# Optimization experiments

Hardware: AMD Instinct MI355X
Metric: run time of the kernel (lower is better)

Reference implementation:

```python
import jax, jax.numpy as jnp
import numpy as np

B = 1024     # number of graphs
NMAX = 128   # max nodes per graph (sizes alternate 128/64 -> total 98304 nodes)
D = 128      # feature dim == UOTPooling.dim
NUM = 4      # Bregman-ADMM iterations
EPS = 1e-8
NEG = -1e9   # masked log-value


def setup_inputs() -> dict:
    key = jax.random.key(0)
    ks = jax.random.split(key, 6)
    sizes = np.where(np.arange(B) % 2 == 0, 128, 64)
    batch = jnp.asarray(np.repeat(np.arange(B), sizes), dtype=jnp.int32)  # (98304,)
    T = int(sizes.sum())
    x = jax.random.normal(ks[0], (T, D), dtype=jnp.float32)
    W1 = jax.random.normal(ks[1], (2 * D, D), dtype=jnp.float32) / np.sqrt(D)
    W2 = jax.random.normal(ks[2], (1, 2 * D), dtype=jnp.float32) / np.sqrt(2 * D)
    a1_raw = 0.1 * jax.random.normal(ks[3], (1, 1), dtype=jnp.float32)
    a2_raw = 0.1 * jax.random.normal(ks[4], (1, 1), dtype=jnp.float32)
    a3_raw = 0.1 * jax.random.normal(ks[5], (1, 1), dtype=jnp.float32)
    return {"x": x, "batch": batch, "W1": W1, "W2": W2,
            "a1_raw": a1_raw, "a2_raw": a2_raw, "a3_raw": a3_raw}


def _segment_softmax(scores, batch):
    # torch_geometric.utils.softmax over ragged segments, numerically stable
    m = jax.ops.segment_max(scores, batch, num_segments=B)
    e = jnp.exp(scores - m[batch])
    s = jax.ops.segment_sum(e, batch, num_segments=B)
    return e / (s[batch] + 1e-16)


def _to_dense_batch(v, batch):
    # scatter flat (T, ...) node values into dense (B, NMAX, ...) + validity mask
    T = v.shape[0]
    counts = jax.ops.segment_sum(jnp.ones((T,), jnp.int32), batch, num_segments=B)
    starts = jnp.cumsum(counts) - counts
    pos = jnp.arange(T, dtype=jnp.int32) - starts[batch]
    dense = jnp.zeros((B, NMAX) + v.shape[1:], v.dtype).at[batch, pos].set(v)
    mask = jnp.zeros((B, NMAX), dtype=bool).at[batch, pos].set(True)
    return dense, mask


def _uot_badmm(xd, p0, q0, a1, a2, a3, mask3):
    # log-domain Bregman-ADMM for entropic unbalanced OT ("badmm-e").
    # T: (B, N, D); row marginal (sum over D) ~ eta (samples), column marginal
    # (sum over N) ~ mu (dims); eta, mu softly tied to priors q0, p0 via KL.
    log_p0 = jnp.log(p0 + EPS)                       # (B, 1, D)
    log_q0 = jnp.log(q0 + EPS)                       # (B, N, 1)
    log_t = jnp.where(mask3, log_q0 + log_p0, NEG)   # (B, N, D)
    log_s = log_t
    log_mu = log_p0                                   # (B, 1, D)
    log_eta = jnp.where(mask3, log_q0, NEG)           # (B, N, 1)
    z = jnp.zeros_like(log_t)
    z1 = jnp.zeros_like(log_mu)
    z2 = jnp.zeros_like(log_eta)
    for _ in range(NUM):
        # T-update: each valid row of T sums to eta (softmax over feature dim)
        y = (xd - z) / a1 + log_s
        log_t = jnp.where(mask3, log_eta + jax.nn.log_softmax(y, axis=2), NEG)
        # S-update: each column of S sums to mu (masked softmax over node dim)
        y = jnp.where(mask3, z / a1 + log_t, NEG)
        log_s = jnp.where(mask3, log_mu + jax.nn.log_softmax(y, axis=1), NEG)
        # closed-form KL-prox updates of the unbalanced marginals
        log_cs = jax.scipy.special.logsumexp(log_s, axis=1, keepdims=True)  # (B,1,D)
        log_mu = (a1 * log_cs + a2 * log_p0 - z1) / (a1 + a2)
        log_rt = jax.scipy.special.logsumexp(log_t, axis=2, keepdims=True)  # (B,N,1)
        log_eta = jnp.where(mask3, (a1 * log_rt + a3 * log_q0 - z2) / (a1 + a3), NEG)
        # dual ascent
        z = z + a1 * (jnp.exp(log_t) - jnp.exp(log_s))
        z1 = z1 + a1 * (jnp.exp(log_mu) - jnp.exp(log_cs))
        z2 = z2 + a1 * (jnp.exp(log_eta) - jnp.exp(log_rt))
    return jnp.exp(log_t)


def reference(x, batch, W1, W2, a1_raw, a2_raw, a3_raw):
    # attention scores -> segment softmax -> sample-marginal prior q0
    scores = jnp.tanh(x @ W1.T) @ W2.T               # (T, 1)
    q0_flat = _segment_softmax(scores, batch)        # (T, 1)
    xd, mask = _to_dense_batch(x, batch)             # (B, NMAX, D), (B, NMAX)
    q0, _ = _to_dense_batch(q0_flat, batch)          # (B, NMAX, 1)
    mask3 = mask[:, :, None]                         # (B, NMAX, 1)
    p0 = jnp.full((B, 1, D), 1.0 / D, dtype=x.dtype)
    a1 = jax.nn.softplus(a1_raw)[0, 0]
    a2 = jax.nn.softplus(a2_raw)[0, 0]
    a3 = jax.nn.softplus(a3_raw)[0, 0]
    trans = _uot_badmm(xd, p0, q0, a1, a2, a3, mask3)  # (B, NMAX, D)
    frot = D * xd * trans * mask3
    return jnp.sum(frot, axis=1)                     # (B, D)
```

## Files before the change

### kernel.cpp

```cpp
#include <hip/hip_runtime.h>
#include <hip/hip_bf16.h>
#include <math.h>

#define NEGC -1000000000.0f

using f32x2 = __attribute__((ext_vector_type(2))) float;
using f32x4 = __attribute__((ext_vector_type(4))) float;
using s16x8 = __attribute__((ext_vector_type(8))) short;

__device__ __forceinline__ float softplusf(float v){ return log1pf(expf(v)); }
__device__ __forceinline__ float frcp(float v){ return __builtin_amdgcn_rcpf(v); }
__device__ __forceinline__ short bfs(float f){
  __hip_bfloat16 h = __float2bfloat16(f);
  short s; __builtin_memcpy(&s, &h, 2); return s;
}

__device__ __forceinline__ float addx32(float v){
#if __has_builtin(__builtin_amdgcn_permlane32_swap)
  auto r = __builtin_amdgcn_permlane32_swap(__float_as_uint(v), __float_as_uint(v), false, false);
  return v + __uint_as_float(r[1]);
#else
  return v + __shfl_xor(v, 32, 64);
#endif
}
__device__ __forceinline__ float addx16(float v){
#if __has_builtin(__builtin_amdgcn_permlane16_swap)
  auto r = __builtin_amdgcn_permlane16_swap(__float_as_uint(v), __float_as_uint(v), false, false);
  return v + __uint_as_float(r[1]);
#else
  return v + __shfl_xor(v, 16, 64);
#endif
}
__device__ __forceinline__ float addx8(float v){
  int s = __builtin_amdgcn_update_dpp(0, __float_as_int(v), 0x128, 0xF, 0xF, true);
  return v + __int_as_float(s);
}
__device__ __forceinline__ float addq1(float v){
  int s = __builtin_amdgcn_update_dpp(0, __float_as_int(v), 0xB1, 0xF, 0xF, true);
  return v + __int_as_float(s);
}
__device__ __forceinline__ float addq2(float v){
  int s = __builtin_amdgcn_update_dpp(0, __float_as_int(v), 0x4E, 0xF, 0xF, true);
  return v + __int_as_float(s);
}

__global__ __launch_bounds__(256) void k_prep(const float* __restrict__ W1,
                                              short* __restrict__ wpack,
                                              const int* __restrict__ batch,
                                              int* __restrict__ starts, int T, int Bn,
                                              int* __restrict__ cnt,
                                              int* __restrict__ bigs,
                                              int* __restrict__ smalls){
  const int bx  = blockIdx.x;
  const int tid = threadIdx.x;
  if (bx < 16){
    int gid  = bx * 256 + tid;
    int lane = gid & 63;
    int ft   = gid >> 6;
    int kt   = ft >> 2;
    int dt   = ft & 3;
    const float* src = W1 + (size_t)(kt * 16 + (lane & 15)) * 128 + dt * 32 + (lane >> 4) * 8;
    short o[8];
#pragma unroll
    for (int e = 0; e < 8; ++e) o[e] = bfs(src[e]);
    *(s16x8*)(wpack + (size_t)gid * 8) = *(const s16x8*)o;
  } else {
    int t = (bx - 16) * 256 + tid;
    if (t > Bn) return;
    int lo = 0, hi = T;
    while (lo < hi){ int mid = (lo + hi) >> 1; if (batch[mid] < t) lo = mid + 1; else hi = mid; }
    if (t == Bn){ starts[Bn] = T; return; }
    starts[t] = lo;
    int lo2 = lo, hi2 = T;
    while (lo2 < hi2){ int mid = (lo2 + hi2) >> 1; if (batch[mid] <= t) lo2 = mid + 1; else hi2 = mid; }
    int nb = lo2 - lo;
    if (nb > 64) bigs[atomicAdd(&cnt[0], 1)] = t;
    else         smalls[atomicAdd(&cnt[1], 1)] = t;
  }
}

__global__ __launch_bounds__(1024)
void k_uot(const float* __restrict__ x,
           const int*   __restrict__ starts,
           const int*   __restrict__ cnt,
           const int*   __restrict__ bigs,
           const int*   __restrict__ smalls,
           const short* __restrict__ wpack,
           const float* __restrict__ W2,
           const float* __restrict__ a1r,
           const float* __restrict__ a2r,
           const float* __restrict__ a3r,
           float* __restrict__ out, int T){
  __shared__ __align__(16) short xs[2 * 64 * 128];
  __shared__ __align__(16) float pbuf[16][164];
  __shared__ float scpart[2][4][64];
  __shared__ float rcsb[2][128];
  __shared__ float lq0s[2][128];
  __shared__ float sred[2][2];

  const int b   = blockIdx.x;
  const int tid = threadIdx.x;
  const int nbig   = cnt[0];
  const int nsmall = cnt[1];

  bool solo; int seg;
  const int half  = tid >> 9;
  const int tid_l = tid & 511;
  if (b < nbig){
    solo = true; seg = bigs[b];
  } else {
    const int i = (b - nbig) * 2 + half;
    solo = false;
    if ((b - nbig) * 2 >= nsmall) return;
    if (i >= nsmall) return;
    seg = smalls[i];
  }

  const int start = starts[seg];
  const int nbr   = starts[seg + 1] - start;
  const int hh    = solo ? 0 : half;
  const int tl    = solo ? tid : tid_l;
  const int PL    = solo ? 8 : 4;

  if (nbr <= 0){
    if (tl < 128) out[(size_t)seg * 128 + tl] = 0.f;
    return;
  }

  const int n    = tl >> 3;
  const int j    = tl & 7;
  const int wvi  = tid >> 6;
  const int lane = tid & 63;
  const int part = tl & (PL - 1);
  const int col  = tl / PL;
  const int cidx = (col >> 4) * 20 + (col & 15);
  const int wq0  = solo ? 0 : half * 8;

  const int u      = tid >> 9;
  const int ustart = solo ? (start + u * 64) : start;
#pragma unroll
  for (int itr = 0; itr < 2; ++itr){
    int L  = (itr * 512 + tid_l) * 8;
    int rr = L >> 7;
    int dc = L & 127;
    int grow = ustart + rr; grow = (grow < T) ? grow : (T - 1);
    const float4 v0 = *(const float4*)(x + (size_t)grow * 128 + dc);
    const float4 v1 = *(const float4*)(x + (size_t)grow * 128 + dc + 4);
    short o[8] = {bfs(v0.x), bfs(v0.y), bfs(v0.z), bfs(v0.w),
                  bfs(v1.x), bfs(v1.y), bfs(v1.z), bfs(v1.w)};
    int byte = u * 16384 + rr * 256 + ((dc * 2) ^ ((rr & 7) << 4));
    *(s16x8*)((char*)xs + byte) = *(const s16x8*)o;
  }
  __syncthreads();

  {
    const int lw = wvi & 7;
    const int wm = lw & 1;
    const int wn = lw >> 1;
    f32x4 acc[2][4];
#pragma unroll
    for (int mt = 0; mt < 2; ++mt)
#pragma unroll
      for (int kt = 0; kt < 4; ++kt) acc[mt][kt] = (f32x4){0.f, 0.f, 0.f, 0.f};

    const s16x8* wp = (const s16x8*)wpack;
#pragma unroll
    for (int dt = 0; dt < 4; ++dt){
      s16x8 av[2];
#pragma unroll
      for (int mt = 0; mt < 2; ++mt){
        int arow = wm * 32 + mt * 16 + (lane & 15);
        int byte = u * 16384 + arow * 256 + ((dt * 64 + (lane >> 4) * 16) ^ ((arow & 7) << 4));
        av[mt] = *(const s16x8*)((const char*)xs + byte);
      }
#pragma unroll
      for (int kt = 0; kt < 4; ++kt){
        s16x8 wv = wp[(size_t)((((wn * 4 + kt) * 4 + dt)) << 6) + lane];
#pragma unroll
        for (int mt = 0; mt < 2; ++mt)
          acc[mt][kt] = __builtin_amdgcn_mfma_f32_16x16x32_bf16(av[mt], wv, acc[mt][kt], 0, 0, 0);
      }
    }

    float psum[2][4] = {{0.f,0.f,0.f,0.f},{0.f,0.f,0.f,0.f}};
#pragma unroll
    for (int kt = 0; kt < 4; ++kt){
      const float w2v  = W2[(wn * 4 + kt) * 16 + (lane & 15)];
      const float w2v2 = w2v + w2v;
#pragma unroll
      for (int mt = 0; mt < 2; ++mt)
#pragma unroll
        for (int r = 0; r < 4; ++r){
          float e = __expf(2.f * acc[mt][kt][r]);
          psum[mt][r] = fmaf(-w2v2, frcp(e + 1.f), psum[mt][r] + w2v);
        }
    }
#pragma unroll
    for (int mt = 0; mt < 2; ++mt)
#pragma unroll
      for (int r = 0; r < 4; ++r){
        float v = psum[mt][r];
        v = addq1(v); v = addq2(v);
        v += __shfl_xor(v, 4, 64); v += __shfl_xor(v, 8, 64);
        if ((lane & 15) == 0)
          scpart[u][wn][wm * 32 + mt * 16 + (lane >> 4) * 4 + r] = v;
      }
  }
  __syncthreads();

  float sc = NEGC;
  if (tl < 128 && tl < nbr){
    const int ru = solo ? (tl >> 6) : hh;
    const int rl = tl & 63;
    sc = scpart[ru][0][rl] + scpart[ru][1][rl] + scpart[ru][2][rl] + scpart[ru][3][rl];
  }
  if (tl < 128) lq0s[hh][tl] = sc;
  if ((wvi & 7) == 0 && (!solo || wvi == 0)){
    float v1 = NEGC;
    const int r2 = lane + 64;
    if (r2 < nbr){
      const int rl2 = r2 & 63;
      v1 = scpart[1][0][rl2] + scpart[1][1][rl2] + scpart[1][2][rl2] + scpart[1][3][rl2];
    }
    float m = fmaxf(sc, v1);
#pragma unroll
    for (int msk = 32; msk; msk >>= 1) m = fmaxf(m, __shfl_xor(m, msk, 64));
    float s = __expf(sc - m) + __expf(v1 - m);
#pragma unroll
    for (int msk = 32; msk; msk >>= 1) s += __shfl_xor(s, msk, 64);
    if (lane == 0){ sred[hh][0] = m; sred[hh][1] = s; }
  }
  __syncthreads();
  const float smax  = sred[hh][0];
  const float rden  = frcp(sred[hh][1] + 1e-16f);
  const bool  valid = (n < nbr);
  const float lq0   = valid ? __logf(__expf(lq0s[hh][n] - smax) * rden + 1e-8f) : NEGC;

  const float a1 = softplusf(a1r[0]);
  const float a2 = softplusf(a2r[0]);
  const float a3 = softplusf(a3r[0]);
  const float inv_a1 = 1.f / a1;
  const float log_p0 = logf(1.0f / 128.0f + 1e-8f);

  float emu_use[3];
  {
    float z1 = 0.f, lp = log_p0;
    emu_use[0] = __expf(log_p0);
#pragma unroll
    for (int i = 1; i < 3; ++i){
      float nm = (a1 * lp + a2 * log_p0 - z1) / (a1 + a2);
      z1 += a1 * (__expf(nm) - __expf(lp));
      emu_use[i] = __expf(nm); lp = nm;
    }
  }
  float eeta_use[4];
  {
    float z2 = 0.f, lp = lq0;
    eeta_use[0] = __expf(lq0);
#pragma unroll
    for (int i = 1; i < 4; ++i){
      float nm = (a1 * lp + a3 * lq0 - z2) / (a1 + a3);
      z2 += a1 * (__expf(nm) - __expf(lp));
      eeta_use[i] = __expf(nm); lp = nm;
    }
  }

  const int  nc   = valid ? n : (nbr - 1);
  const float* xp = x + (size_t)(start + nc) * 128 + j * 16;
  f32x2 EX2[8], PZ2[8], S2[8];
  {
    const float s0 = __expf(lq0 + log_p0);
#pragma unroll
    for (int p = 0; p < 8; p += 2){
      float4 v = *(const float4*)(xp + p * 2);
      EX2[p]   = (f32x2){__expf(v.x * inv_a1), __expf(v.y * inv_a1)};
      EX2[p+1] = (f32x2){__expf(v.z * inv_a1), __expf(v.w * inv_a1)};
    }
#pragma unroll
    for (int p = 0; p < 8; ++p){ PZ2[p] = (f32x2){1.f, 1.f}; S2[p] = (f32x2){s0, s0}; }
  }

#pragma unroll
  for (int it = 0; it < 4; ++it){
    f32x2 ES2[8];
    f32x2 rs2 = (f32x2){0.f, 0.f};
#pragma unroll
    for (int p = 0; p < 8; ++p){
      ES2[p] = EX2[p] * S2[p];
      rs2 += ES2[p] * PZ2[p];
    }
    float rsum = rs2[0] + rs2[1];
    rsum = addq1(rsum);
    rsum = addq2(rsum);
    rsum += __shfl_xor(rsum, 4, 64);
    const float Et = valid ? (eeta_use[it] * frcp(rsum)) : 0.f;
    const f32x2 Et2 = (f32x2){Et, Et};

    if (it == 3){
      float c[16];
#pragma unroll
      for (int p = 0; p < 8; p += 2){
        float4 v = *(const float4*)(xp + p * 2);
        f32x2 t0 = ES2[p]   * PZ2[p]   * Et2;
        f32x2 t1 = ES2[p+1] * PZ2[p+1] * Et2;
        c[p*2+0] = v.x * t0[0]; c[p*2+1] = v.y * t0[1];
        c[p*2+2] = v.z * t1[0]; c[p*2+3] = v.w * t1[1];
      }
#pragma unroll
      for (int k = 0; k < 16; ++k)
        c[k] = addx8(addx16(addx32(c[k])));
      if (lane < 8){
        float* p = &pbuf[wvi][lane * 20];
        *(float4*)(p + 0)  = make_float4(c[0],  c[1],  c[2],  c[3]);
        *(float4*)(p + 4)  = make_float4(c[4],  c[5],  c[6],  c[7]);
        *(float4*)(p + 8)  = make_float4(c[8],  c[9],  c[10], c[11]);
        *(float4*)(p + 12) = make_float4(c[12], c[13], c[14], c[15]);
      }
      __syncthreads();
      {
        float s = pbuf[wq0 + part][cidx] + pbuf[wq0 + part + PL][cidx];
        s = addq2(addq1(s));
        if (PL == 8) s += __shfl_xor(s, 4, 64);
        if (part == 0) out[(size_t)seg * 128 + col] = 128.f * s;
      }
    } else {
      const float emu = emu_use[it];
      float c[16];
#pragma unroll
      for (int p = 0; p < 8; ++p){
        f32x2 e2 = ES2[p] * Et2;
        c[p*2+0] = e2[0]; c[p*2+1] = e2[1];
      }
#pragma unroll
      for (int k = 0; k < 16; ++k)
        c[k] = addx8(addx16(addx32(c[k])));
      if (lane < 8){
        float* p = &pbuf[wvi][lane * 20];
        *(float4*)(p + 0)  = make_float4(c[0],  c[1],  c[2],  c[3]);
        *(float4*)(p + 4)  = make_float4(c[4],  c[5],  c[6],  c[7]);
        *(float4*)(p + 8)  = make_float4(c[8],  c[9],  c[10], c[11]);
        *(float4*)(p + 12) = make_float4(c[12], c[13], c[14], c[15]);
      }
      __syncthreads();
      {
        float s = pbuf[wq0 + part][cidx] + pbuf[wq0 + part + PL][cidx];
        s = addq2(addq1(s));
        if (PL == 8) s += __shfl_xor(s, 4, 64);
        if (part == 0) rcsb[hh][col] = emu * frcp(fmaxf(s, 1e-30f));
      }
      __syncthreads();
      f32x2 rc2[8];
      {
        const float4 r0 = *(const float4*)&rcsb[hh][j * 16 + 0];
        const float4 r1 = *(const float4*)&rcsb[hh][j * 16 + 4];
        const float4 r2 = *(const float4*)&rcsb[hh][j * 16 + 8];
        const float4 r3 = *(const float4*)&rcsb[hh][j * 16 + 12];
        rc2[0] = (f32x2){r0.x, r0.y}; rc2[1] = (f32x2){r0.z, r0.w};
        rc2[2] = (f32x2){r1.x, r1.y}; rc2[3] = (f32x2){r1.z, r1.w};
        rc2[4] = (f32x2){r2.x, r2.y}; rc2[5] = (f32x2){r2.z, r2.w};
        rc2[6] = (f32x2){r3.x, r3.y}; rc2[7] = (f32x2){r3.z, r3.w};
      }
#pragma unroll
      for (int p = 0; p < 8; ++p){
        f32x2 e2  = ES2[p] * Et2;
        f32x2 sn  = e2 * rc2[p];
        f32x2 arg = e2 * (rc2[p] - PZ2[p]);
        PZ2[p] *= (f32x2){__expf(arg[0]), __expf(arg[1])};
        S2[p] = sn;
      }
    }
  }
}

extern "C" void kernel_launch(void* const* d_in, const int* in_sizes, int n_in,
                              void* d_out, int out_size, void* d_ws, size_t ws_size,
                              hipStream_t stream){
  const float* x    = (const float*)d_in[0];
  const int*   batch= (const int*)  d_in[1];
  const float* W1   = (const float*)d_in[2];
  const float* W2   = (const float*)d_in[3];
  const float* a1r  = (const float*)d_in[4];
  const float* a2r  = (const float*)d_in[5];
  const float* a3r  = (const float*)d_in[6];
  float* out = (float*)d_out;

  const int T  = in_sizes[1];
  const int Bn = out_size / 128;

  short* wpack  = (short*)d_ws;
  int*   starts = (int*)(wpack + 32768);
  int*   cnt    = starts + (Bn + 2);
  int*   bigs   = cnt + 2;
  int*   smalls = bigs + Bn;

  hipMemsetAsync(cnt, 0, 2 * sizeof(int), stream);
  const int segBlocks = (Bn + 256) / 256;
  k_prep<<<16 + segBlocks, 256, 0, stream>>>(W1, wpack, batch, starts, T, Bn,
                                             cnt, bigs, smalls);
  k_uot<<<Bn, 1024, 0, stream>>>(x, starts, cnt, bigs, smalls, wpack, W2,
                                 a1r, a2r, a3r, out, T);
}
```

Measured before the change: 81.79 us.

## Replace memset and atomic segment classification with single-block scan; use DPP row reductions

Segment-boundary search and big/small classification move into one block. It runs interleaved binary searches, then does a shared-memory prefix scan to assign list positions deterministically instead of using atomics. This removes the hipMemsetAsync launch and the atomic counters. Several xor-4/xor-8 shuffles become DPP row_half_mirror/row_mirror adds, which avoids ds_swizzle/bpermute latency. The mirror patterns give the same sums within a row only when all lanes are being reduced symmetrically, and the single-block prep caps at 2048 segments.

```diff
diff --git a/kernel.cpp b/kernel.cpp
--- a/kernel.cpp
+++ b/kernel.cpp
@@ -41,6 +41,14 @@
 }
 __device__ __forceinline__ float addq2(float v){
   int s = __builtin_amdgcn_update_dpp(0, __float_as_int(v), 0x4E, 0xF, 0xF, true);
+  return v + __int_as_float(s);
+}
+__device__ __forceinline__ float addrhm(float v){
+  int s = __builtin_amdgcn_update_dpp(0, __float_as_int(v), 0x141, 0xF, 0xF, true);
+  return v + __int_as_float(s);
+}
+__device__ __forceinline__ float addrm(float v){
+  int s = __builtin_amdgcn_update_dpp(0, __float_as_int(v), 0x140, 0xF, 0xF, true);
   return v + __int_as_float(s);
 }
 
@@ -64,18 +72,60 @@
 #pragma unroll
     for (int e = 0; e < 8; ++e) o[e] = bfs(src[e]);
     *(s16x8*)(wpack + (size_t)gid * 8) = *(const s16x8*)o;
-  } else {
-    int t = (bx - 16) * 256 + tid;
-    if (t > Bn) return;
-    int lo = 0, hi = T;
-    while (lo < hi){ int mid = (lo + hi) >> 1; if (batch[mid] < t) lo = mid + 1; else hi = mid; }
-    if (t == Bn){ starts[Bn] = T; return; }
-    starts[t] = lo;
-    int lo2 = lo, hi2 = T;
-    while (lo2 < hi2){ int mid = (lo2 + hi2) >> 1; if (batch[mid] <= t) lo2 = mid + 1; else hi2 = mid; }
-    int nb = lo2 - lo;
-    if (nb > 64) bigs[atomicAdd(&cnt[0], 1)] = t;
-    else         smalls[atomicAdd(&cnt[1], 1)] = t;
+    return;
+  }
+  __shared__ int sstart[2049];
+  __shared__ int scn[256];
+  int lo[8], hi[8];
+  int ns = 0;
+  for (int t = tid; t <= Bn; t += 256){ if (ns < 8){ lo[ns] = 0; hi[ns] = T; } ns++; }
+  if (ns > 8) ns = 8;
+  for (int step = 0; step < 24; ++step){
+#pragma unroll
+    for (int q = 0; q < 8; ++q){
+      if (q < ns && lo[q] < hi[q]){
+        int t   = tid + (q << 8);
+        int mid = (lo[q] + hi[q]) >> 1;
+        if (batch[mid] < t) lo[q] = mid + 1; else hi[q] = mid;
+      }
+    }
+  }
+#pragma unroll
+  for (int q = 0; q < 8; ++q) if (q < ns){
+    int t = tid + (q << 8);
+    starts[t] = lo[q];
+    if (t <= 2048) sstart[t] = lo[q];
+  }
+  __syncthreads();
+  const int ck = (Bn + 255) >> 8;
+  const int s0 = tid * ck;
+  int myb = 0; unsigned flags = 0;
+#pragma unroll
+  for (int q = 0; q < 8; ++q){
+    int s = s0 + q;
+    if (q < ck && s < Bn){
+      int nb = sstart[s + 1] - sstart[s];
+      if (nb > 64){ flags |= (1u << q); myb++; }
+    }
+  }
+  scn[tid] = myb;
+  __syncthreads();
+  for (int off = 1; off < 256; off <<= 1){
+    int v = scn[tid];
+    int w = (tid >= off) ? scn[tid - off] : 0;
+    __syncthreads();
+    scn[tid] = v + w;
+    __syncthreads();
+  }
+  int bposs = scn[tid] - myb;
+  if (tid == 255){ cnt[0] = scn[255]; cnt[1] = Bn - scn[255]; }
+#pragma unroll
+  for (int q = 0; q < 8; ++q){
+    int s = s0 + q;
+    if (q < ck && s < Bn){
+      if (flags & (1u << q)){ bigs[bposs] = s; bposs++; }
+      else                  { smalls[s - bposs] = s; }
+    }
   }
 }
 
@@ -201,7 +251,8 @@
       for (int r = 0; r < 4; ++r){
         float v = psum[mt][r];
         v = addq1(v); v = addq2(v);
-        v += __shfl_xor(v, 4, 64); v += __shfl_xor(v, 8, 64);
+        v = addrhm(v);
+        v = addrm(v);
         if ((lane & 15) == 0)
           scpart[u][wn][wm * 32 + mt * 16 + (lane >> 4) * 4 + r] = v;
       }
@@ -292,7 +343,7 @@
     float rsum = rs2[0] + rs2[1];
     rsum = addq1(rsum);
     rsum = addq2(rsum);
-    rsum += __shfl_xor(rsum, 4, 64);
+    rsum = addrhm(rsum);
     const float Et = valid ? (eeta_use[it] * frcp(rsum)) : 0.f;
     const f32x2 Et2 = (f32x2){Et, Et};
 
@@ -320,7 +371,7 @@
       {
         float s = pbuf[wq0 + part][cidx] + pbuf[wq0 + part + PL][cidx];
         s = addq2(addq1(s));
-        if (PL == 8) s += __shfl_xor(s, 4, 64);
+        if (PL == 8) s = addrhm(s);
         if (part == 0) out[(size_t)seg * 128 + col] = 128.f * s;
       }
     } else {
@@ -345,7 +396,7 @@
       {
         float s = pbuf[wq0 + part][cidx] + pbuf[wq0 + part + PL][cidx];
         s = addq2(addq1(s));
-        if (PL == 8) s += __shfl_xor(s, 4, 64);
+        if (PL == 8) s = addrhm(s);
         if (part == 0) rcsb[hh][col] = emu * frcp(fmaxf(s, 1e-30f));
       }
       __syncthreads();
@@ -393,10 +444,8 @@
   int*   bigs   = cnt + 2;
   int*   smalls = bigs + Bn;
 
-  hipMemsetAsync(cnt, 0, 2 * sizeof(int), stream);
-  const int segBlocks = (Bn + 256) / 256;
-  k_prep<<<16 + segBlocks, 256, 0, stream>>>(W1, wpack, batch, starts, T, Bn,
-                                             cnt, bigs, smalls);
+  k_prep<<<17, 256, 0, stream>>>(W1, wpack, batch, starts, T, Bn,
+                                 cnt, bigs, smalls);
   k_uot<<<Bn, 1024, 0, stream>>>(x, starts, cnt, bigs, smalls, wpack, W2,
                                  a1r, a2r, a3r, out, T);
 }
```

New measurement: 91.76 us. 12.2% more time.
